# Kernel tuning notes

Measured on AMD Instinct MI355X. Metric: run time of the kernel, lower is better.

The kernel has to match this reference:

```python
import jax, jax.numpy as jnp
import numpy as np

B, C, H, W = 4, 128, 256, 256
N_KPTS = 2048
N_POS = 8
KS = 3
CH = 2 * N_POS  # channel_num (mask=False)


def setup_inputs() -> dict:
    key = jax.random.key(0)
    ks = jax.random.split(key, 8)
    x = jax.random.normal(ks[0], (B, C, H, W), jnp.float32)
    keypoints = jax.random.uniform(ks[1], (B, N_KPTS, 2), jnp.float32, -1.0, 1.0)
    s1 = 1.0 / np.sqrt(C * KS * KS)
    W1 = jax.random.uniform(ks[2], (CH, C, KS, KS), jnp.float32, -s1, s1)
    b1 = jax.random.uniform(ks[3], (CH,), jnp.float32, -s1, s1)
    s2 = 1.0 / np.sqrt(CH)
    W2 = jax.random.uniform(ks[4], (CH, CH), jnp.float32, -s2, s2)
    b2 = jax.random.uniform(ks[5], (CH,), jnp.float32, -s2, s2)
    s3 = 1.0 / np.sqrt(C)
    sf_w = jax.random.uniform(ks[6], (C, C), jnp.float32, -s3, s3)
    agg_w = jax.random.uniform(ks[7], (N_POS, C, C), jnp.float32)  # torch.rand
    return {"x": x, "keypoints": keypoints, "W1": W1, "b1": b1,
            "W2": W2, "b2": b2, "sf_w": sf_w, "agg_w": agg_w}


def _bilinear(img, px, py):
    """grid_sample(bilinear, align_corners=True, padding=zeros) in pixel coords.
    img: [c,h,w]; px,py: [M] -> [c,M]."""
    h, w = img.shape[1], img.shape[2]
    x0f = jnp.floor(px); y0f = jnp.floor(py)
    x0 = x0f.astype(jnp.int32); y0 = y0f.astype(jnp.int32)
    wx1 = px - x0f; wy1 = py - y0f
    wx0 = 1.0 - wx1; wy0 = 1.0 - wy1

    def tap(yi, xi, wgt):
        valid = (xi >= 0) & (xi < w) & (yi >= 0) & (yi < h)
        v = img[:, jnp.clip(yi, 0, h - 1), jnp.clip(xi, 0, w - 1)]
        return v * (wgt * valid)[None]

    return (tap(y0, x0, wy0 * wx0) + tap(y0, x0 + 1, wy0 * wx1)
            + tap(y0 + 1, x0, wy1 * wx0) + tap(y0 + 1, x0 + 1, wy1 * wx1))


def reference(x, keypoints, W1, b1, W2, b2, sf_w, agg_w):
    wh = jnp.array([W - 1, H - 1], jnp.float32)
    max_off = max(H, W) / 4.0
    taps = jnp.arange(KS)

    def per_image(xi, kpts):
        kwh = (kpts / 2.0 + 0.5) * wh                     # [N,2] pixel coords (x,y)
        rc = kwh.astype(jnp.int32)                        # .long() trunc (coords >= 0)
        # corner = trunc(rc - ps/2 + 1) then clamp -> rc-1 clamped (ps=3)
        lim = jnp.array([W - 1 - KS, H - 1 - KS])
        corner = jnp.clip(rc - 1, 0, lim)                 # [N,2] (x,y)
        rows = corner[:, 1, None] + taps                  # [N,ks]
        cols = corner[:, 0, None] + taps                  # [N,ks]
        patch = xi[:, rows[:, :, None], cols[:, None, :]] # [c,N,ks,ks]
        patch = patch.transpose(1, 0, 2, 3)               # [N,c,ks,ks]
        # offset_conv: 3x3 conv (valid, ->1x1) + ReLU + 1x1 conv
        h1 = jax.nn.relu(jnp.einsum('ncab,ocab->no', patch, W1) + b1)
        off = h1 @ W2.T + b2                              # [N,2*n_pos]
        off = jnp.clip(off, -max_off, max_off)
        offset = off.reshape(-1, 2, N_POS).transpose(0, 2, 1)  # [N,n_pos,2]
        pos = kwh[:, None, :] + offset                    # [N,n_pos,2] pixel coords
        # 2*pos/wh - 1 then align_corners unnormalize == pos
        feat = _bilinear(xi, pos[..., 0].reshape(-1), pos[..., 1].reshape(-1))  # [c,N*p]
        feat = feat.reshape(C, -1, N_POS).transpose(1, 0, 2)  # [N,c,p]
        feat = jax.nn.selu(jnp.einsum('oc,ncp->nop', sf_w, feat))
        descs = jnp.einsum('ncp,pcd->nd', feat, agg_w)    # [N,dims]
        nrm = jnp.maximum(jnp.linalg.norm(descs, axis=1, keepdims=True), 1e-12)
        return descs / nrm, offset

    descriptors, offsets = jax.vmap(per_image)(x, keypoints)
    return descriptors, offsets
```

## Files before the change

### kernel.cpp

```cpp
#include <hip/hip_runtime.h>
#include <hip/hip_bf16.h>
#include <math.h>

#define B_ 4
#define C_ 128
#define H_ 256
#define W_ 256
#define NK 2048
#define NP 8
#define HW_ (H_*W_)
#define MAXOFF 64.0f
#define NROWS (B_*NK)

typedef short s16x8 __attribute__((ext_vector_type(8)));
typedef short s16x4 __attribute__((ext_vector_type(4)));
typedef float f32x4 __attribute__((ext_vector_type(4)));

#define SELU_SC 1.0507009873554805f
#define SELU_AL 1.6732632423543772f

#define N_W1F (36*64*8)
#define N_SFB (8*4*64*8)
#define N_AGG (8*8*4*64*8)
#define NPREP (N_W1F + N_SFB + N_AGG)
#define NT_BLK (B_*HW_/64)
#define NP_BLK 81
#define LSTR 136

__device__ inline float bf2f(short b) {
    union { unsigned int u; float f; } cv;
    cv.u = ((unsigned int)(unsigned short)b) << 16;
    return cv.f;
}
__device__ inline short f2bf_s(float f) {
    __hip_bfloat16 h = __float2bfloat16(f);
    return *(short*)&h;
}

__global__ __launch_bounds__(256) void k_transpose_prep(const float* __restrict__ x,
        __hip_bfloat16* __restrict__ xt,
        const float* __restrict__ W1, const float* __restrict__ sf_w,
        const float* __restrict__ agg_w,
        __hip_bfloat16* __restrict__ w1f, __hip_bfloat16* __restrict__ sfb,
        __hip_bfloat16* __restrict__ aggb) {
    __shared__ __align__(16) __hip_bfloat16 lt[64*LSTR];
    int bid = blockIdx.x;
    int t = threadIdx.x;
    if (bid >= NT_BLK) {
        int base = ((bid - NT_BLK)*256 + t)*8;
        #pragma unroll
        for (int j = 0; j < 8; ++j) {
            int u0 = base + j;
            if (u0 < N_W1F) {
                int e = u0 & 7, l = (u0 >> 3) & 63, ks = u0 >> 9;
                int o = l & 15, c = (ks & 3)*32 + ((l >> 4) << 3) + e, ab = ks >> 2;
                w1f[u0] = __float2bfloat16(W1[o*1152 + c*9 + ab]);
            } else if (u0 < N_W1F + N_SFB) {
                int u = u0 - N_W1F;
                int e = u & 7, l = (u >> 3) & 63, ks = (u >> 9) & 3, jj = u >> 11;
                sfb[u] = __float2bfloat16(sf_w[(jj*16 + (l & 15))*128 + ks*32 + ((l >> 4) << 3) + e]);
            } else if (u0 < NPREP) {
                int u = u0 - N_W1F - N_SFB;
                int e = u & 7, l = (u >> 3) & 63, ks = (u >> 9) & 3, p = (u >> 11) & 7, jd = u >> 14;
                aggb[u] = __float2bfloat16(agg_w[((size_t)p*128 + ks*32 + ((l >> 4) << 3) + e)*128 + jd*16 + (l & 15)]);
            }
        }
        return;
    }
    int i = bid >> 10;
    int hw0 = (bid & 1023) * 64;
    const float* src = x + (size_t)i*C_*HW_ + hw0;
    #pragma unroll
    for (int k = 0; k < 8; ++k) {
        int f = t + k*256;
        int c = f >> 4, hq = f & 15;
        float4 v = *(const float4*)(src + (size_t)c*HW_ + hq*4);
        int hw = hq*4;
        lt[(hw+0)*LSTR + c] = __float2bfloat16(v.x);
        lt[(hw+1)*LSTR + c] = __float2bfloat16(v.y);
        lt[(hw+2)*LSTR + c] = __float2bfloat16(v.z);
        lt[(hw+3)*LSTR + c] = __float2bfloat16(v.w);
    }
    __syncthreads();
    __hip_bfloat16* dst = xt + ((size_t)i*HW_ + hw0)*C_;
    #pragma unroll
    for (int k = 0; k < 4; ++k) {
        int e = t + k*256;
        int hw = e >> 4, c0 = (e & 15)*8;
        *(s16x8*)(dst + (size_t)hw*C_ + c0) = *(const s16x8*)&lt[hw*LSTR + c0];
    }
}

#define FSTR 1032
#define HSTR 136
#define RSTR 132
__global__ __launch_bounds__(256, 4) void k_fused(
        const __hip_bfloat16* __restrict__ xtb, const float* __restrict__ kpts,
        const __hip_bfloat16* __restrict__ w1f, const float* __restrict__ b1,
        const float* __restrict__ W2, const float* __restrict__ b2,
        const __hip_bfloat16* __restrict__ sfb, const __hip_bfloat16* __restrict__ aggb,
        float* __restrict__ out_off, float* __restrict__ descs) {
    __shared__ __align__(16) char smem[33792];
    __shared__ float W2s[16][16];
    __shared__ float posL[16][8][2];
    __shared__ float kwx[16], kwy[16];
    __shared__ int   kcx[16], kcy[16];

    int t = threadIdx.x;
    int blk = blockIdx.x;
    int i = blk >> 7;
    int w = t >> 6, l = t & 63;
    int r16 = l & 15, q = l >> 4;
    int kp0 = blk * 16;

    if (t < 16) {
        int gk = kp0 + t;
        float kx = kpts[(size_t)gk*2], ky = kpts[(size_t)gk*2 + 1];
        float wx = (kx*0.5f + 0.5f) * (float)(W_-1);
        float wy = (ky*0.5f + 0.5f) * (float)(H_-1);
        int cx = (int)wx - 1; cx = min(max(cx, 0), W_-1-3);
        int cy = (int)wy - 1; cy = min(max(cy, 0), H_-1-3);
        kwx[t] = wx; kwy[t] = wy; kcx[t] = cx; kcy[t] = cy;
    }
    W2s[t >> 4][t & 15] = W2[t];
    __syncthreads();

    float* Cp  = (float*)smem;
    float* hLr = (float*)(smem + 4352);
    {
        const char* pb = (const char*)(xtb +
            ((size_t)(i*H_ + kcy[r16])*W_ + kcx[r16])*C_);
        f32x4 acc = {0.f, 0.f, 0.f, 0.f};
        #pragma unroll
        for (int s = 0; s < 9; ++s) {
            int ks = w*9 + s;
            int ab = ks >> 2;
            int a = ab/3, b = ab - (ab/3)*3;
            int off = ((a*W_ + b)*C_ + (ks & 3)*32 + q*8) * 2;
            s16x8 af = *(const s16x8*)(pb + off);
            s16x8 bf = *(const s16x8*)((const short*)w1f + ((size_t)ks*64 + l)*8);
            acc = __builtin_amdgcn_mfma_f32_16x16x32_bf16(af, bf, acc, 0, 0, 0);
        }
        #pragma unroll
        for (int r = 0; r < 4; ++r)
            Cp[(w*16 + q*4 + r)*17 + r16] = acc[r];
    }
    __syncthreads();
    {
        int kp = t >> 4, o = t & 15;
        float sum = Cp[(0*16 + kp)*17 + o] + Cp[(1*16 + kp)*17 + o]
                  + Cp[(2*16 + kp)*17 + o] + Cp[(3*16 + kp)*17 + o];
        hLr[kp*17 + o] = fmaxf(sum + b1[o], 0.f);
        __syncthreads();
        float acc2 = b2[o];
        #pragma unroll
        for (int oo = 0; oo < 16; ++oo)
            acc2 += hLr[kp*17 + oo] * W2s[o][oo];
        acc2 = fminf(fmaxf(acc2, -MAXOFF), MAXOFF);
        int d = o >> 3, p = o & 7;
        int gk = kp0 + kp;
        out_off[((size_t)gk*NP + p)*2 + d] = acc2;
        posL[kp][p][d] = (d ? kwy[kp] : kwx[kp]) + acc2;
    }
    __syncthreads();

    __hip_bfloat16* featL = (__hip_bfloat16*)smem;
    {
        int half = t >> 5, lane32 = t & 31;
        int c0 = lane32 * 4;
        #pragma unroll 4
        for (int s = 0; s < 16; ++s) {
            int pr = s*8 + half;
            int kp = pr >> 3, p = pr & 7;
            float px = posL[kp][p][0], py = posL[kp][p][1];
            float x0f = floorf(px), y0f = floorf(py);
            int x0 = (int)x0f, y0 = (int)y0f;
            float wx1 = px - x0f, wy1 = py - y0f;
            float wx0 = 1.f - wx1, wy0 = 1.f - wy1;
            float a0 = 0.f, a1 = 0.f, a2 = 0.f, a3 = 0.f;
            #pragma unroll
            for (int tap = 0; tap < 4; ++tap) {
                int xi = x0 + (tap & 1);
                int yi = y0 + (tap >> 1);
                float wgt = ((tap & 1) ? wx1 : wx0) * ((tap >> 1) ? wy1 : wy0);
                bool valid = (xi >= 0) & (xi < W_) & (yi >= 0) & (yi < H_);
                int xc = min(max(xi, 0), W_-1);
                int yc = min(max(yi, 0), H_-1);
                float wv = valid ? wgt : 0.f;
                const __hip_bfloat16* src = xtb + ((size_t)(i*H_ + yc)*W_ + xc)*C_ + c0;
                s16x4 v = *(const s16x4*)src;
                a0 += wv * bf2f(v[0]);
                a1 += wv * bf2f(v[1]);
                a2 += wv * bf2f(v[2]);
                a3 += wv * bf2f(v[3]);
            }
            s16x4 ov;
            ov[0] = f2bf_s(a0); ov[1] = f2bf_s(a1);
            ov[2] = f2bf_s(a2); ov[3] = f2bf_s(a3);
            *(s16x4*)(featL + kp*FSTR + p*C_ + c0) = ov;
        }
    }
    __syncthreads();

    s16x8 af[2][4];
    #pragma unroll
    for (int pi = 0; pi < 2; ++pi) {
        int p = w*2 + pi;
        #pragma unroll
        for (int ks = 0; ks < 4; ++ks)
            af[pi][ks] = *(const s16x8*)(featL + r16*FSTR + p*C_ + ks*32 + q*8);
    }
    __syncthreads();

    __hip_bfloat16* Hl = (__hip_bfloat16*)(smem + (size_t)w*4352);
    f32x4 dacc[8];
    #pragma unroll
    for (int jd = 0; jd < 8; ++jd) dacc[jd] = (f32x4){0.f,0.f,0.f,0.f};
    #pragma unroll
    for (int pi = 0; pi < 2; ++pi) {
        int p = w*2 + pi;
        #pragma unroll
        for (int j = 0; j < 8; ++j) {
            f32x4 acc = (f32x4){0.f,0.f,0.f,0.f};
            const short* sb = (const short*)sfb + ((j*4)*64 + l)*8;
            #pragma unroll
            for (int ks = 0; ks < 4; ++ks)
                acc = __builtin_amdgcn_mfma_f32_16x16x32_bf16(af[pi][ks], *(const s16x8*)(sb + ks*512), acc, 0, 0, 0);
            #pragma unroll
            for (int r = 0; r < 4; ++r) {
                float v = acc[r];
                v = v > 0.f ? SELU_SC*v : SELU_SC*SELU_AL*(__expf(v) - 1.0f);
                Hl[(q*4 + r)*HSTR + j*16 + r16] = __float2bfloat16(v);
            }
        }
        s16x8 ah[4];
        #pragma unroll
        for (int ks = 0; ks < 4; ++ks)
            ah[ks] = *(const s16x8*)(Hl + r16*HSTR + ks*32 + q*8);
        #pragma unroll
        for (int jd = 0; jd < 8; ++jd) {
            const short* ab = (const short*)aggb + (((jd*8 + p)*4)*64 + l)*8;
            #pragma unroll
            for (int ks = 0; ks < 4; ++ks)
                dacc[jd] = __builtin_amdgcn_mfma_f32_16x16x32_bf16(ah[ks], *(const s16x8*)(ab + ks*512), dacc[jd], 0, 0, 0);
        }
    }
    __syncthreads();

    float* red = (float*)smem;
    #pragma unroll
    for (int jd = 0; jd < 8; ++jd)
        #pragma unroll
        for (int r = 0; r < 4; ++r)
            red[((size_t)w*16 + q*4 + r)*RSTR + jd*16 + r16] = dacc[jd][r];
    __syncthreads();

    {
        int row = t >> 4, c0 = t & 15;
        float v[8];
        float ss = 0.f;
        #pragma unroll
        for (int k = 0; k < 8; ++k) {
            int col = c0 + 16*k;
            float s = red[(0*16 + row)*RSTR + col] + red[(1*16 + row)*RSTR + col]
                    + red[(2*16 + row)*RSTR + col] + red[(3*16 + row)*RSTR + col];
            v[k] = s; ss += s*s;
        }
        ss += __shfl_xor(ss, 1);
        ss += __shfl_xor(ss, 2);
        ss += __shfl_xor(ss, 4);
        ss += __shfl_xor(ss, 8);
        float sc = fmaxf(sqrtf(ss), 1e-12f);
        #pragma unroll
        for (int k = 0; k < 8; ++k)
            descs[(size_t)(kp0 + row)*C_ + c0 + 16*k] = v[k] / sc;
    }
}

__global__ __launch_bounds__(64) void k_offsets_f32(const float* __restrict__ xin,
        const float* __restrict__ kpts, const float* __restrict__ W1,
        const float* __restrict__ b1, const float* __restrict__ W2,
        const float* __restrict__ b2, float* __restrict__ out_off,
        float* __restrict__ pos) {
    __shared__ float pL[1152];
    __shared__ float hL2[16];
    __shared__ float oL[16];
    int bid = blockIdx.x;
    int i = bid >> 11;
    int t = threadIdx.x;
    float kx = kpts[(size_t)bid*2 + 0];
    float ky = kpts[(size_t)bid*2 + 1];
    float kwhx = (kx*0.5f + 0.5f) * (float)(W_-1);
    float kwhy = (ky*0.5f + 0.5f) * (float)(H_-1);
    int cx = (int)kwhx - 1; cx = cx < 0 ? 0 : (cx > 252 ? 252 : cx);
    int cy = (int)kwhy - 1; cy = cy < 0 ? 0 : (cy > 252 ? 252 : cy);
    for (int e = t; e < 1152; e += 64) {
        int a = e/384; int r = e - a*384; int b = r >> 7; int c = r & 127;
        pL[e] = xin[(((size_t)(i*C_ + c))*H_ + cy + a)*W_ + cx + b];
    }
    __syncthreads();
    int o = t & 15;
    int chunk = t >> 4;
    float partial = 0.f;
    const float* w1r = W1 + o*1152;
    for (int c = chunk*32; c < chunk*32 + 32; ++c) {
        #pragma unroll
        for (int ab = 0; ab < 9; ++ab) {
            const int a = ab/3, b = ab - (ab/3)*3;
            partial += w1r[c*9 + ab] * pL[a*384 + b*128 + c];
        }
    }
    partial += __shfl_xor(partial, 16);
    partial += __shfl_xor(partial, 32);
    float h1 = fmaxf(partial + b1[o], 0.f);
    if (t < 16) hL2[t] = h1;
    __syncthreads();
    if (t < 16) {
        float acc = b2[t];
        const float* w2r = W2 + t*16;
        #pragma unroll
        for (int oo = 0; oo < 16; ++oo) acc += w2r[oo]*hL2[oo];
        acc = fminf(fmaxf(acc, -MAXOFF), MAXOFF);
        oL[t] = acc;
    }
    __syncthreads();
    if (t < 8) {
        float ox = oL[t], oy = oL[8 + t];
        size_t base = ((size_t)bid*NP + t)*2;
        out_off[base]   = ox;
        out_off[base+1] = oy;
        pos[base]   = kwhx + ox;
        pos[base+1] = kwhy + oy;
    }
}

__global__ __launch_bounds__(128) void k_sample_f32(const float* __restrict__ xin,
        const float* __restrict__ pos, const float* __restrict__ sf_w,
        const float* __restrict__ agg_w, float* __restrict__ dst) {
    __shared__ __align__(16) float featL[NP*C_];
    __shared__ float pp[16];
    int bid = blockIdx.x;
    int i = bid >> 11;
    int c = threadIdx.x;
    if (c < 16) pp[c] = pos[(size_t)bid*16 + c];
    __syncthreads();
    #pragma unroll
    for (int p = 0; p < NP; ++p) {
        float px = pp[p*2], py = pp[p*2+1];
        float x0f = floorf(px), y0f = floorf(py);
        int x0 = (int)x0f, y0 = (int)y0f;
        float wx1 = px - x0f, wy1 = py - y0f;
        float wx0 = 1.f - wx1, wy0 = 1.f - wy1;
        float acc = 0.f;
        #pragma unroll
        for (int tap = 0; tap < 4; ++tap) {
            int xi = x0 + (tap & 1);
            int yi = y0 + (tap >> 1);
            float w = ((tap & 1) ? wx1 : wx0) * ((tap >> 1) ? wy1 : wy0);
            bool valid = (xi >= 0) & (xi < W_) & (yi >= 0) & (yi < H_);
            int xc = min(max(xi, 0), W_-1);
            int yc = min(max(yi, 0), H_-1);
            acc += (valid ? w : 0.f) * xin[(((size_t)(i*C_ + c))*H_ + yc)*W_ + xc];
        }
        featL[p*C_ + c] = acc;
    }
    __syncthreads();
    float acc[NP];
    #pragma unroll
    for (int p = 0; p < NP; ++p) acc[p] = 0.f;
    const float4* sfr = (const float4*)(sf_w + (size_t)c*C_);
    const float4* fL4 = (const float4*)featL;
    for (int c4 = 0; c4 < C_/4; ++c4) {
        float4 wv = sfr[c4];
        #pragma unroll
        for (int p = 0; p < NP; ++p) {
            float4 f = fL4[p*(C_/4) + c4];
            acc[p] += wv.x*f.x + wv.y*f.y + wv.z*f.z + wv.w*f.w;
        }
    }
    #pragma unroll
    for (int p = 0; p < NP; ++p) {
        float v = acc[p];
        acc[p] = v > 0.f ? SELU_SC*v : SELU_SC*SELU_AL*(__expf(v) - 1.0f);
    }
    __shared__ __align__(16) float gL[NP*C_];
    #pragma unroll
    for (int p = 0; p < NP; ++p) gL[p*C_ + c] = acc[p];
    __syncthreads();
    float d_acc = 0.f;
    for (int pc = 0; pc < NP*C_; ++pc)
        d_acc += gL[pc] * agg_w[(size_t)pc*C_ + c];
    dst[(size_t)bid*C_ + c] = d_acc;
}

__global__ __launch_bounds__(64) void k_norm(float* __restrict__ out) {
    int row = blockIdx.x;
    int l = threadIdx.x;
    float* r = out + (size_t)row*C_;
    float a = r[l], b = r[l+64];
    float ss = a*a + b*b;
    #pragma unroll
    for (int m = 1; m < 64; m <<= 1) ss += __shfl_xor(ss, m);
    float s = fmaxf(sqrtf(ss), 1e-12f);
    r[l] = a/s; r[l+64] = b/s;
}

extern "C" void kernel_launch(void* const* d_in, const int* in_sizes, int n_in,
                              void* d_out, int out_size, void* d_ws, size_t ws_size,
                              hipStream_t stream) {
    const float* x    = (const float*)d_in[0];
    const float* kpts = (const float*)d_in[1];
    const float* W1   = (const float*)d_in[2];
    const float* b1   = (const float*)d_in[3];
    const float* W2   = (const float*)d_in[4];
    const float* b2   = (const float*)d_in[5];
    const float* sfw  = (const float*)d_in[6];
    const float* aggw = (const float*)d_in[7];
    float* out_desc = (float*)d_out;
    float* out_off  = out_desc + (size_t)B_*NK*C_;

    char* ws = (char*)d_ws;
    float* pos = (float*)ws;
    const size_t W1F_OFF = (size_t)1 << 20;
    const size_t SFB_OFF = (size_t)2 << 20;
    const size_t AGG_OFF = (size_t)3 << 20;
    const size_t XT_OFF  = (size_t)1 << 26;
    const size_t XT_BYTES = (size_t)B_*H_*W_*C_*2;
    bool useXT = ws_size >= XT_OFF + XT_BYTES;
    __hip_bfloat16* xtb  = (__hip_bfloat16*)(ws + XT_OFF);
    __hip_bfloat16* w1f  = (__hip_bfloat16*)(ws + W1F_OFF);
    __hip_bfloat16* sfb  = (__hip_bfloat16*)(ws + SFB_OFF);
    __hip_bfloat16* aggb = (__hip_bfloat16*)(ws + AGG_OFF);

    if (useXT) {
        k_transpose_prep<<<NT_BLK + NP_BLK, 256, 0, stream>>>(x, xtb, W1, sfw, aggw,
                                                              w1f, sfb, aggb);
        k_fused<<<NROWS/16, 256, 0, stream>>>(xtb, kpts, w1f, b1, W2, b2, sfb, aggb,
                                              out_off, out_desc);
    } else {
        k_offsets_f32<<<NROWS, 64, 0, stream>>>(x, kpts, W1, b1, W2, b2, out_off, pos);
        k_sample_f32<<<NROWS, 128, 0, stream>>>(x, pos, sfw, aggw, out_desc);
        k_norm<<<NROWS, 64, 0, stream>>>(out_desc);
    }
}
```

Baseline: 62.35 us.

## Double fused kernel block to 512 threads and redistribute work across eight waves

Launches the fused kernel with 512 threads (eight waves) instead of 256. The 36 conv K-steps are split 5/4 across the eight waves and reduced from eight partials. Sampling now takes half as many iterations per thread, and each wave handles one sampling position instead of two. Descriptor partials are combined in two phases through shared memory. The intent is more latency hiding and parallelism per keypoint tile, since the grid has only 512 blocks. The costs are extra synchronisation and reduction steps, plus register pressure under the new launch bounds.

Result: faster. 59.28 us (-4.9%).

```diff
diff --git a/kernel.cpp b/kernel.cpp
--- a/kernel.cpp
+++ b/kernel.cpp
@@ -94,13 +94,14 @@
 #define FSTR 1032
 #define HSTR 136
 #define RSTR 132
-__global__ __launch_bounds__(256, 4) void k_fused(
+#define SMEM_BYTES 34816
+__global__ __launch_bounds__(512, 4) void k_fused(
         const __hip_bfloat16* __restrict__ xtb, const float* __restrict__ kpts,
         const __hip_bfloat16* __restrict__ w1f, const float* __restrict__ b1,
         const float* __restrict__ W2, const float* __restrict__ b2,
         const __hip_bfloat16* __restrict__ sfb, const __hip_bfloat16* __restrict__ aggb,
         float* __restrict__ out_off, float* __restrict__ descs) {
-    __shared__ __align__(16) char smem[33792];
+    __shared__ __align__(16) char smem[SMEM_BYTES];
     __shared__ float W2s[16][16];
     __shared__ float posL[16][8][2];
     __shared__ float kwx[16], kwy[16];
@@ -122,18 +123,19 @@
         int cy = (int)wy - 1; cy = min(max(cy, 0), H_-1-3);
         kwx[t] = wx; kwy[t] = wy; kcx[t] = cx; kcy[t] = cy;
     }
-    W2s[t >> 4][t & 15] = W2[t];
+    if (t < 256) W2s[t >> 4][t & 15] = W2[t];
     __syncthreads();
 
     float* Cp  = (float*)smem;
-    float* hLr = (float*)(smem + 4352);
+    float* hLr = (float*)(smem + 8704);
     {
         const char* pb = (const char*)(xtb +
             ((size_t)(i*H_ + kcy[r16])*W_ + kcx[r16])*C_);
         f32x4 acc = {0.f, 0.f, 0.f, 0.f};
-        #pragma unroll
-        for (int s = 0; s < 9; ++s) {
-            int ks = w*9 + s;
+        int nst  = (w < 4) ? 5 : 4;
+        int kbase = (w < 4) ? w*5 : 20 + (w-4)*4;
+        for (int s = 0; s < nst; ++s) {
+            int ks = kbase + s;
             int ab = ks >> 2;
             int a = ab/3, b = ab - (ab/3)*3;
             int off = ((a*W_ + b)*C_ + (ks & 3)*32 + q*8) * 2;
@@ -146,12 +148,17 @@
             Cp[(w*16 + q*4 + r)*17 + r16] = acc[r];
     }
     __syncthreads();
-    {
+    if (t < 256) {
         int kp = t >> 4, o = t & 15;
-        float sum = Cp[(0*16 + kp)*17 + o] + Cp[(1*16 + kp)*17 + o]
-                  + Cp[(2*16 + kp)*17 + o] + Cp[(3*16 + kp)*17 + o];
+        float sum = 0.f;
+        #pragma unroll
+        for (int ww = 0; ww < 8; ++ww)
+            sum += Cp[(ww*16 + kp)*17 + o];
         hLr[kp*17 + o] = fmaxf(sum + b1[o], 0.f);
-        __syncthreads();
+    }
+    __syncthreads();
+    if (t < 256) {
+        int kp = t >> 4, o = t & 15;
         float acc2 = b2[o];
         #pragma unroll
         for (int oo = 0; oo < 16; ++oo)
@@ -166,11 +173,11 @@
 
     __hip_bfloat16* featL = (__hip_bfloat16*)smem;
     {
-        int half = t >> 5, lane32 = t & 31;
+        int grp = t >> 5, lane32 = t & 31;
         int c0 = lane32 * 4;
-        #pragma unroll 4
-        for (int s = 0; s < 16; ++s) {
-            int pr = s*8 + half;
+        #pragma unroll
+        for (int s = 0; s < 8; ++s) {
+            int pr = s*16 + grp;
             int kp = pr >> 3, p = pr & 7;
             float px = posL[kp][p][0], py = posL[kp][p][1];
             float x0f = floorf(px), y0f = floorf(py);
@@ -202,14 +209,11 @@
     }
     __syncthreads();
 
-    s16x8 af[2][4];
-    #pragma unroll
-    for (int pi = 0; pi < 2; ++pi) {
-        int p = w*2 + pi;
-        #pragma unroll
-        for (int ks = 0; ks < 4; ++ks)
-            af[pi][ks] = *(const s16x8*)(featL + r16*FSTR + p*C_ + ks*32 + q*8);
-    }
+    int p = w;
+    s16x8 af[4];
+    #pragma unroll
+    for (int ks = 0; ks < 4; ++ks)
+        af[ks] = *(const s16x8*)(featL + r16*FSTR + p*C_ + ks*32 + q*8);
     __syncthreads();
 
     __hip_bfloat16* Hl = (__hip_bfloat16*)(smem + (size_t)w*4352);
@@ -217,51 +221,59 @@
     #pragma unroll
     for (int jd = 0; jd < 8; ++jd) dacc[jd] = (f32x4){0.f,0.f,0.f,0.f};
     #pragma unroll
-    for (int pi = 0; pi < 2; ++pi) {
-        int p = w*2 + pi;
-        #pragma unroll
-        for (int j = 0; j < 8; ++j) {
-            f32x4 acc = (f32x4){0.f,0.f,0.f,0.f};
-            const short* sb = (const short*)sfb + ((j*4)*64 + l)*8;
+    for (int j = 0; j < 8; ++j) {
+        f32x4 acc = (f32x4){0.f,0.f,0.f,0.f};
+        const short* sb = (const short*)sfb + ((j*4)*64 + l)*8;
+        #pragma unroll
+        for (int ks = 0; ks < 4; ++ks)
+            acc = __builtin_amdgcn_mfma_f32_16x16x32_bf16(af[ks], *(const s16x8*)(sb + ks*512), acc, 0, 0, 0);
+        #pragma unroll
+        for (int r = 0; r < 4; ++r) {
+            float v = acc[r];
+            v = v > 0.f ? SELU_SC*v : SELU_SC*SELU_AL*(__expf(v) - 1.0f);
+            Hl[(q*4 + r)*HSTR + j*16 + r16] = __float2bfloat16(v);
+        }
+    }
+    s16x8 ah[4];
+    #pragma unroll
+    for (int ks = 0; ks < 4; ++ks)
+        ah[ks] = *(const s16x8*)(Hl + r16*HSTR + ks*32 + q*8);
+    #pragma unroll
+    for (int jd = 0; jd < 8; ++jd) {
+        const short* ab = (const short*)aggb + (((jd*8 + p)*4)*64 + l)*8;
+        #pragma unroll
+        for (int ks = 0; ks < 4; ++ks)
+            dacc[jd] = __builtin_amdgcn_mfma_f32_16x16x32_bf16(ah[ks], *(const s16x8*)(ab + ks*512), dacc[jd], 0, 0, 0);
+    }
+    __syncthreads();
+
+    float* red = (float*)smem;
+    if (w < 4) {
+        #pragma unroll
+        for (int jd = 0; jd < 8; ++jd)
             #pragma unroll
-            for (int ks = 0; ks < 4; ++ks)
-                acc = __builtin_amdgcn_mfma_f32_16x16x32_bf16(af[pi][ks], *(const s16x8*)(sb + ks*512), acc, 0, 0, 0);
+            for (int r = 0; r < 4; ++r)
+                red[((size_t)w*16 + q*4 + r)*RSTR + jd*16 + r16] = dacc[jd][r];
+    }
+    __syncthreads();
+    if (w >= 4) {
+        #pragma unroll
+        for (int jd = 0; jd < 8; ++jd)
             #pragma unroll
             for (int r = 0; r < 4; ++r) {
-                float v = acc[r];
-                v = v > 0.f ? SELU_SC*v : SELU_SC*SELU_AL*(__expf(v) - 1.0f);
-                Hl[(q*4 + r)*HSTR + j*16 + r16] = __float2bfloat16(v);
+                size_t idx = ((size_t)(w-4)*16 + q*4 + r)*RSTR + jd*16 + r16;
+                red[idx] += dacc[jd][r];
             }
-        }
-        s16x8 ah[4];
-        #pragma unroll
-        for (int ks = 0; ks < 4; ++ks)
-            ah[ks] = *(const s16x8*)(Hl + r16*HSTR + ks*32 + q*8);
-        #pragma unroll
-        for (int jd = 0; jd < 8; ++jd) {
-            const short* ab = (const short*)aggb + (((jd*8 + p)*4)*64 + l)*8;
-            #pragma unroll
-            for (int ks = 0; ks < 4; ++ks)
-                dacc[jd] = __builtin_amdgcn_mfma_f32_16x16x32_bf16(ah[ks], *(const s16x8*)(ab + ks*512), dacc[jd], 0, 0, 0);
-        }
-    }
-    __syncthreads();
-
-    float* red = (float*)smem;
-    #pragma unroll
-    for (int jd = 0; jd < 8; ++jd)
-        #pragma unroll
-        for (int r = 0; r < 4; ++r)
-            red[((size_t)w*16 + q*4 + r)*RSTR + jd*16 + r16] = dacc[jd][r];
+    }
     __syncthreads();
 
     {
-        int row = t >> 4, c0 = t & 15;
-        float v[8];
+        int row = t >> 5, c5 = t & 31;
+        float v[4];
         float ss = 0.f;
         #pragma unroll
-        for (int k = 0; k < 8; ++k) {
-            int col = c0 + 16*k;
+        for (int k = 0; k < 4; ++k) {
+            int col = c5 + 32*k;
             float s = red[(0*16 + row)*RSTR + col] + red[(1*16 + row)*RSTR + col]
                     + red[(2*16 + row)*RSTR + col] + red[(3*16 + row)*RSTR + col];
             v[k] = s; ss += s*s;
@@ -270,10 +282,11 @@
         ss += __shfl_xor(ss, 2);
         ss += __shfl_xor(ss, 4);
         ss += __shfl_xor(ss, 8);
+        ss += __shfl_xor(ss, 16);
         float sc = fmaxf(sqrtf(ss), 1e-12f);
         #pragma unroll
-        for (int k = 0; k < 8; ++k)
-            descs[(size_t)(kp0 + row)*C_ + c0 + 16*k] = v[k] / sc;
+        for (int k = 0; k < 4; ++k)
+            descs[(size_t)(kp0 + row)*C_ + c5 + 32*k] = v[k] / sc;
     }
 }
 
@@ -435,7 +448,7 @@
     if (useXT) {
         k_transpose_prep<<<NT_BLK + NP_BLK, 256, 0, stream>>>(x, xtb, W1, sfw, aggw,
                                                               w1f, sfb, aggb);
-        k_fused<<<NROWS/16, 256, 0, stream>>>(xtb, kpts, w1f, b1, W2, b2, sfb, aggb,
+        k_fused<<<NROWS/16, 512, 0, stream>>>(xtb, kpts, w1f, b1, W2, b2, sfb, aggb,
                                               out_off, out_desc);
     } else {
         k_offsets_f32<<<NROWS, 64, 0, stream>>>(x, kpts, W1, b1, W2, b2, out_off, pos);
```
